# Kernel optimization log

Measured on AMD Instinct MI355X. Metric: run time of the kernel, lower is better.

## Reference

```python
import jax, jax.numpy as jnp
import numpy as np

B, T, F, H = 64, 1024, 512, 512


def setup_inputs() -> dict:
    key = jax.random.key(0)
    k1, k2, k3 = jax.random.split(key, 3)
    scale_x = 1.0 / np.sqrt(F)
    scale_h = 1.0 / np.sqrt(H)
    inputs = jax.random.normal(k1, (B, T, F), dtype=jnp.float32)
    Wx = jax.random.normal(k2, (F, 4 * H), dtype=jnp.float32) * scale_x
    Wh = jax.random.normal(k3, (H, 4 * H), dtype=jnp.float32) * scale_h
    # flax LSTMCell inits forget-gate bias to ones, others zero (gate order i,f,g,o)
    b = jnp.concatenate([jnp.zeros((H,)), jnp.ones((H,)), jnp.zeros((2 * H,))]).astype(jnp.float32)
    return {"inputs": inputs, "Wx": Wx, "Wh": Wh, "b": b}


def reference(inputs, Wx, Wh, b):
    """LSTM encoder: scan LSTMCell over time, return final carry (c, h).

    inputs: [B, T, F]; Wx: [F, 4H]; Wh: [H, 4H]; b: [4H].
    Gate order i, f, g, o (matches flax.nn.LSTMCell).
    """
    Bx = inputs.shape[0]
    Hh = Wh.shape[0]
    # Precompute input projections for all timesteps in one big GEMM: [T, B, 4H]
    x_proj = jnp.einsum('btf,fg->tbg', inputs, Wx) + b

    def step(carry, xp_t):
        c, h = carry
        gates = xp_t + h @ Wh  # [B, 4H]
        i, f, g, o = jnp.split(gates, 4, axis=-1)
        i = jax.nn.sigmoid(i)
        f = jax.nn.sigmoid(f)
        g = jnp.tanh(g)
        o = jax.nn.sigmoid(o)
        c_new = f * c + i * g
        h_new = o * jnp.tanh(c_new)
        return (c_new, h_new), None

    c0 = jnp.zeros((Bx, Hh), dtype=inputs.dtype)
    h0 = jnp.zeros((Bx, Hh), dtype=inputs.dtype)
    (c_fin, h_fin), _ = jax.lax.scan(step, (c0, h0), x_proj)
    return c_fin, h_fin
```

## Files before the change

kernel.cpp:

```cpp
#include <hip/hip_runtime.h>
#include <hip/hip_fp16.h>

#define T_DIM 1024
#define B_DIM 64
#define F_DIM 512
#define H_DIM 512
#define G4    2048
#define HSZ   (B_DIM*H_DIM)

typedef _Float16 h16;
typedef unsigned long long u64;
typedef _Float16 v8h __attribute__((ext_vector_type(8)));
typedef _Float16 v4h __attribute__((ext_vector_type(4)));
typedef _Float16 v2h __attribute__((ext_vector_type(2)));
typedef float    v4f __attribute__((ext_vector_type(4)));
typedef unsigned v4u __attribute__((ext_vector_type(4)));
typedef unsigned v2u __attribute__((ext_vector_type(2)));

#define NGRP   8
#define GROWS  8
#define GWORDS 2048
#define NWG    128
#define DESC_OFF  ((size_t)2*NGRP*GWORDS)
#define TRIAL_OFF (DESC_OFF + NWG)
#define VOTE_OFF  (TRIAL_OFF + NWG)
#define ABORT_OFF (VOTE_OFF + NWG)

#define XP_HALVES ((size_t)T_DIM * 256 * 2 * 64 * 4)
#define XP_BYTES  (XP_HALVES * 2)
#define HB_WORDS  (ABORT_OFF + NGRP)
#define HB_BYTES  (HB_WORDS * 8)
#define X16_BYTES ((size_t)B_DIM * T_DIM * F_DIM * 2)
#define WXP_BYTES ((size_t)G4 * F_DIM * 2)

__global__ __launch_bounds__(256) void conv_x_kernel(
    const float* __restrict__ X, h16* __restrict__ X16)
{
  const size_t total4 = (size_t)B_DIM * T_DIM * F_DIM / 4;
  for (size_t i = blockIdx.x * 256 + threadIdx.x; i < total4;
       i += (size_t)gridDim.x * 256) {
    float4 v = ((const float4*)X)[i];
    v4h w = { (h16)v.x, (h16)v.y, (h16)v.z, (h16)v.w };
    ((v4h*)X16)[i] = w;
  }
}

__global__ __launch_bounds__(256) void conv_w_kernel(
    const float* __restrict__ Wx, h16* __restrict__ Wxp)
{
  const int gid = blockIdx.x * 256 + threadIdx.x;
  const int pcg = gid >> 6;
  const int k8  = gid & 63;
  const int ub  = pcg >> 5, Tt = (pcg >> 4) & 1, nn = pcg & 15;
  const int gcol = (Tt*2 + (nn >> 3))*512 + ub*8 + (nn & 7);
  v8h w;
  #pragma unroll
  for (int j = 0; j < 8; ++j)
    w[j] = (h16)Wx[(size_t)(k8*8 + j)*G4 + gcol];
  *(v8h*)(Wxp + (size_t)pcg*512 + k8*8) = w;
}

__global__ __launch_bounds__(256) void xproj_kernel(
    const h16* __restrict__ X16, const h16* __restrict__ Wxp,
    const float* __restrict__ bias, h16* __restrict__ xp)
{
  __shared__ __align__(16) h16 As[128*72];
  __shared__ __align__(16) h16 Bs[128*72];
  const int wgid = blockIdx.x;
  const int wgn  = wgid & 15;
  const int bg   = (wgid >> 4) & 3;
  const int t0   = (wgid >> 6) * 8;
  const int tid  = threadIdx.x;
  const int lane = tid & 63;
  const int wv   = tid >> 6;
  const int mh   = wv & 1, nh = wv >> 1;
  const int n    = lane & 15, quad = lane >> 4;

  v4f acc[4][4];
  #pragma unroll
  for (int mi = 0; mi < 4; ++mi)
    #pragma unroll
    for (int ni = 0; ni < 4; ++ni) acc[mi][ni] = {0.f, 0.f, 0.f, 0.f};

  const int m  = tid >> 1;
  const int kh = tid & 1;
  const int abl = m & 15, atl = m >> 4;
  const h16* asrc0 = X16 + ((size_t)(bg*16 + abl)*T_DIM + (t0 + atl))*F_DIM
                         + kh*32;
  const h16* bsrc0 = Wxp + (size_t)(wgn*128 + m)*512 + kh*32;
  h16* adst = As + m*72 + kh*32;
  h16* bdst = Bs + m*72 + kh*32;

  for (int kc = 0; kc < 8; ++kc) {
    __syncthreads();
    {
      const h16* asrc = asrc0 + kc*64;
      const h16* bsrc = bsrc0 + kc*64;
      #pragma unroll
      for (int j = 0; j < 32; j += 8) {
        *(v8h*)(adst + j) = *(const v8h*)(asrc + j);
        *(v8h*)(bdst + j) = *(const v8h*)(bsrc + j);
      }
    }
    __syncthreads();
    #pragma unroll
    for (int kk = 0; kk < 2; ++kk) {
      v8h aF[4], bF[4];
      #pragma unroll
      for (int mi = 0; mi < 4; ++mi)
        aF[mi] = *(const v8h*)(As + ((mh*4 + mi)*16 + n)*72 + kk*32 + quad*8);
      #pragma unroll
      for (int ni = 0; ni < 4; ++ni)
        bF[ni] = *(const v8h*)(Bs + ((nh*4 + ni)*16 + n)*72 + kk*32 + quad*8);
      #pragma unroll
      for (int mi = 0; mi < 4; ++mi)
        #pragma unroll
        for (int ni = 0; ni < 4; ++ni)
          acc[mi][ni] = __builtin_amdgcn_mfma_f32_16x16x32_f16(
              aF[mi], bF[ni], acc[mi][ni], 0, 0, 0);
    }
  }
  #pragma unroll
  for (int ni = 0; ni < 4; ++ni) {
    int pc0  = wgn*128 + (nh*4 + ni)*16;
    int ub   = pc0 >> 5, Tt = (pc0 >> 4) & 1;
    int gcol = (Tt*2 + (n >> 3))*512 + ub*8 + (n & 7);
    float bv = bias[gcol];
    int wg2  = bg*64 + ub;
    #pragma unroll
    for (int mi = 0; mi < 4; ++mi) {
      int t = t0 + mh*4 + mi;
      size_t off = ((((size_t)t*256 + wg2)*2 + Tt)*256) + lane*4;
      v4h o = { (h16)(acc[mi][ni][0] + bv), (h16)(acc[mi][ni][1] + bv),
                (h16)(acc[mi][ni][2] + bv), (h16)(acc[mi][ni][3] + bv) };
      *(v4h*)(xp + off) = o;
    }
  }
}

__device__ __forceinline__ float fsig(float x) {
  return __builtin_amdgcn_rcpf(1.f + __expf(-x));
}
__device__ __forceinline__ float ftanh(float x) {
  return 1.f - 2.f * __builtin_amdgcn_rcpf(__expf(2.f*x) + 1.f);
}

__device__ __forceinline__ u64 load_nt_u64(const u64* p) {
  v2u r;
  asm volatile("global_load_dwordx2 %0, %1, off nt\n\ts_waitcnt vmcnt(0)"
               : "=v"(r) : "v"(p) : "memory");
  return ((u64)r.y << 32) | (u64)r.x;
}

__global__ __launch_bounds__(256, 1) void scan_kernel(
    const float* __restrict__ Wh, const h16* __restrict__ xp,
    u64* __restrict__ hbuf, float* __restrict__ out)
{
  const int bx   = blockIdx.x;
  const int tid  = threadIdx.x;
  const int wv   = tid >> 6;
  const int lane = tid & 63;
  const int n    = lane & 15, quad = lane >> 4;

  __shared__ __align__(16) unsigned hlds[2][2052];
  __shared__ float gbuf[4][16*33];
  __shared__ unsigned char xcds[NWG];
  __shared__ unsigned char pos2bx[NWG];
  __shared__ int sflag[2];

  unsigned xcd;
  asm volatile("s_getreg_b32 %0, hwreg(20, 0, 32)" : "=s"(xcd));
  xcd &= 7u;
  u64* const desc = hbuf + DESC_OFF;
  if (tid == 0)
    __hip_atomic_store(desc + bx, ((u64)0xABu << 56) | (u64)xcd,
                       __ATOMIC_RELAXED, __HIP_MEMORY_SCOPE_AGENT);
  if (tid < NWG) {
    u64 d = __hip_atomic_load(desc + tid, __ATOMIC_RELAXED,
                              __HIP_MEMORY_SCOPE_AGENT);
    while ((unsigned)(d >> 56) != 0xABu) {
      __builtin_amdgcn_s_sleep(1);
      d = __hip_atomic_load(desc + tid, __ATOMIC_RELAXED,
                            __HIP_MEMORY_SCOPE_AGENT);
    }
    xcds[tid] = (unsigned char)(d & 7u);
  }
  if (tid < 4) { hlds[0][2048 + tid] = 0; hlds[1][2048 + tid] = 0; }
  __syncthreads();

  int start = 0, cnt = 0, rank = 0;
  for (int i = 0; i < NWG; ++i) {
    const int x = xcds[i];
    start += (x < (int)xcd) ? 1 : 0;
    cnt   += (x == (int)xcd) ? 1 : 0;
    rank  += (x == (int)xcd && i < bx) ? 1 : 0;
  }
  const int pos = start + rank;
  const int g = pos >> 4, w = pos & 15;
  bool fast = (g*16 >= start) && (g*16 + 16 <= start + cnt);

  if (fast) {
    if (tid < NWG) {
      const int xi = xcds[tid];
      int st = 0, rk = 0;
      for (int i = 0; i < NWG; ++i) {
        const int x = xcds[i];
        st += (x < xi) ? 1 : 0;
        rk += (x == xi && i < tid) ? 1 : 0;
      }
      pos2bx[st + rk] = (unsigned char)tid;
    }
    __syncthreads();
    u64* const trial = hbuf + TRIAL_OFF;
    u64* const vote  = hbuf + VOTE_OFF;
    if (tid == 0)
      __hip_atomic_store(trial + bx, ((u64)0xCDu << 56) | (u64)bx,
                         __ATOMIC_RELAXED, __HIP_MEMORY_SCOPE_WORKGROUP);
    int seen = 1;
    if (tid < 16) {
      const int tb = pos2bx[g*16 + tid];
      const u64 want = ((u64)0xCDu << 56) | (u64)tb;
      seen = 0;
      for (int it = 0; it < 1024; ++it) {
        if (load_nt_u64(trial + tb) == want) { seen = 1; break; }
        __builtin_amdgcn_s_sleep(1);
      }
    }
    if (tid < 64) {
      const int okw = __all(seen);
      if (tid == 0) sflag[0] = okw;
    }
    __syncthreads();
    if (tid == 0)
      __hip_atomic_store(vote + bx, ((u64)0xEFu << 56) | (u64)(sflag[0] & 1),
                         __ATOMIC_RELAXED, __HIP_MEMORY_SCOPE_AGENT);
    int vok = 1;
    if (tid < 16) {
      const int tb = pos2bx[g*16 + tid];
      u64 d = __hip_atomic_load(vote + tb, __ATOMIC_RELAXED,
                                __HIP_MEMORY_SCOPE_AGENT);
      while ((unsigned)(d >> 56) != 0xEFu) {
        __builtin_amdgcn_s_sleep(1);
        d = __hip_atomic_load(vote + tb, __ATOMIC_RELAXED,
                              __HIP_MEMORY_SCOPE_AGENT);
      }
      vok = (int)(d & 1);
    }
    if (tid < 64) {
      const int allv = __all(vok);
      if (tid == 0) sflag[1] = allv;
    }
    __syncthreads();
    fast = (sflag[1] != 0);
  }

  const int ub  = w*4 + wv;
  const int u0  = ub*8;
  const int g01 = n >> 3;
  const int uc  = u0 + (n & 7);

  v8h bF0[16], bF1[16];
  #pragma unroll
  for (int kk = 0; kk < 16; ++kk) {
    const int kb = kk*32 + quad*8;
    v8h f0, f1;
    #pragma unroll
    for (int j = 0; j < 8; ++j) {
      f0[j] = (h16)Wh[(size_t)(kb + j)*G4 + (g01*512 + uc)];
      f1[j] = (h16)Wh[(size_t)(kb + j)*G4 + ((2 + g01)*512 + uc)];
    }
    bF0[kk] = f0; bF1[kk] = f1;
  }

  float c0 = 0.f, c1 = 0.f, hf0 = 0.f, hf1 = 0.f;

  const bool act = (n < GROWS);
  const int  pW  = ub*32 + n*4 + quad;
  u64* const gbase0 = hbuf + (size_t)g * GWORDS;
  u64* const gbase1 = hbuf + (size_t)(NGRP + g) * GWORDS;
  u64* const abw    = hbuf + ABORT_OFF + g;
  u64* const gb0p   = gbase0 + pW;
  u64* const gb1p   = gbase1 + pW;
  u64 lw0 = 0, lw1 = 0;

  const int bgrp  = g >> 1;
  const int qq    = (g & 1)*2 + (quad & 1);
  const int lanep = n + 16*qq;
  size_t xoff = ((size_t)(bgrp*64 + ub)*2)*256 + lanep*4;
  v4h x0 = *(const v4h*)(xp + xoff);
  v4h x1 = *(const v4h*)(xp + xoff + 256);

  const int hbase = act ? (quad*32 + n*4) : 2048;
  const int hoff  = act ? 128 : 0;

  for (int t = 0; t < T_DIM; ++t) {
    const int p = t & 1;
    v4h nx0 = x0, nx1 = x1;
    const bool pre = (t + 1 < T_DIM);
    bool did_pre = false;
    const size_t nxo = (((size_t)(t+1)*256 + bgrp*64 + ub)*2)*256 + lanep*4;
    if (!fast && pre) {
      nx0 = *(const v4h*)(xp + nxo);
      nx1 = *(const v4h*)(xp + nxo + 256);
      did_pre = true;
    }

    u64* const hb = (p ? gbase1 : gbase0) + tid*2;
    const unsigned target = (unsigned)t;
    unsigned pay0, pay1, pay2, pay3, pay4, pay5, pay6, pay7;
    bool got = false;

    if (fast) {
      const u64* a0 = hb;
      const u64* a1 = hb + 512;
      const u64* a2 = hb + 1024;
      const u64* a3 = hb + 1536;
      int rounds = 0;
      for (;;) {
        v4u q0, q1, q2, q3;
        asm volatile("global_load_dwordx4 %0, %1, off nt"
                     : "=v"(q0) : "v"(a0) : "memory");
        asm volatile("global_load_dwordx4 %0, %1, off nt"
                     : "=v"(q1) : "v"(a1) : "memory");
        asm volatile("global_load_dwordx4 %0, %1, off nt"
                     : "=v"(q2) : "v"(a2) : "memory");
        asm volatile("global_load_dwordx4 %0, %1, off nt"
                     : "=v"(q3) : "v"(a3) : "memory");
        asm volatile("s_waitcnt vmcnt(0)"
                     : "+v"(q0), "+v"(q1), "+v"(q2), "+v"(q3) :: "memory");
        __builtin_amdgcn_sched_barrier(0);
        const unsigned bad = (q0.y ^ target) | (q0.w ^ target)
                           | (q1.y ^ target) | (q1.w ^ target)
                           | (q2.y ^ target) | (q2.w ^ target)
                           | (q3.y ^ target) | (q3.w ^ target);
        if (__all((int)(bad == 0))) {
          pay0 = q0.x; pay1 = q0.z; pay2 = q1.x; pay3 = q1.z;
          pay4 = q2.x; pay5 = q2.z; pay6 = q3.x; pay7 = q3.z;
          got = true;
          break;
        }
        ++rounds;
        if ((rounds & 31) == 16) {
          u64 ab = __hip_atomic_load(abw, __ATOMIC_RELAXED,
                                     __HIP_MEMORY_SCOPE_AGENT);
          if (__any((int)(ab != 0)) || rounds > 512) {
            __hip_atomic_store(abw, (u64)1, __ATOMIC_RELAXED,
                               __HIP_MEMORY_SCOPE_AGENT);
            if (lw0) __hip_atomic_store(gb0p, lw0, __ATOMIC_RELAXED,
                                        __HIP_MEMORY_SCOPE_AGENT);
            if (lw1) __hip_atomic_store(gb1p, lw1, __ATOMIC_RELAXED,
                                        __HIP_MEMORY_SCOPE_AGENT);
            fast = false;
            break;
          }
        }
        __builtin_amdgcn_s_sleep(1);
      }
    }
    if (!got) {
      for (;;) {
        u64 wq[8];
        #pragma unroll
        for (int j = 0; j < 4; ++j) {
          wq[j*2]   = __hip_atomic_load(hb + j*512,     __ATOMIC_RELAXED,
                                        __HIP_MEMORY_SCOPE_AGENT);
          wq[j*2+1] = __hip_atomic_load(hb + j*512 + 1, __ATOMIC_RELAXED,
                                        __HIP_MEMORY_SCOPE_AGENT);
        }
        unsigned bad = 0;
        #pragma unroll
        for (int j = 0; j < 8; ++j)
          bad |= ((unsigned)(wq[j] >> 32)) ^ target;
        if (__all((int)(bad == 0))) {
          pay0 = (unsigned)wq[0]; pay1 = (unsigned)wq[1];
          pay2 = (unsigned)wq[2]; pay3 = (unsigned)wq[3];
          pay4 = (unsigned)wq[4]; pay5 = (unsigned)wq[5];
          pay6 = (unsigned)wq[6]; pay7 = (unsigned)wq[7];
          break;
        }
        __builtin_amdgcn_s_sleep(1);
      }
    }

    {
      v2u* hl = (v2u*)hlds[p];
      hl[tid]       = (v2u){pay0, pay1};
      hl[tid + 256] = (v2u){pay2, pay3};
      hl[tid + 512] = (v2u){pay4, pay5};
      hl[tid + 768] = (v2u){pay6, pay7};
    }
    __syncthreads();

    if (pre && !did_pre) {
      nx0 = *(const v4h*)(xp + nxo);
      nx1 = *(const v4h*)(xp + nxo + 256);
    }

    v4f acc0 = { (float)x0[0], (float)x0[1], (float)x0[2], (float)x0[3] };
    v4f acc1 = { (float)x1[0], (float)x1[1], (float)x1[2], (float)x1[3] };
    v4f acc2 = { 0.f, 0.f, 0.f, 0.f };
    v4f acc3 = { 0.f, 0.f, 0.f, 0.f };
    const unsigned* hfr = &hlds[p][hbase];
    #pragma unroll
    for (int kk = 0; kk < 8; ++kk) {
      v8h a0 = *(const v8h*)(hfr + kk*hoff);
      v8h a1 = *(const v8h*)(hfr + (kk+8)*hoff);
      acc0 = __builtin_amdgcn_mfma_f32_16x16x32_f16(a0, bF0[kk],   acc0, 0,0,0);
      acc1 = __builtin_amdgcn_mfma_f32_16x16x32_f16(a0, bF1[kk],   acc1, 0,0,0);
      acc2 = __builtin_amdgcn_mfma_f32_16x16x32_f16(a1, bF0[kk+8], acc2, 0,0,0);
      acc3 = __builtin_amdgcn_mfma_f32_16x16x32_f16(a1, bF1[kk+8], acc3, 0,0,0);
    }
    acc0 += acc2; acc1 += acc3;

    float* gb = gbuf[wv];
    #pragma unroll
    for (int r = 0; r < 4; ++r) {
      const int row = quad*4 + r;
      gb[row*33 + n]      = acc0[r];
      gb[row*33 + 16 + n] = acc1[r];
    }
    __builtin_amdgcn_wave_barrier();
    const float* gr = gb + n*33;
    const int ua2 = quad*2;
    float gi0 = gr[ua2],   gf0 = gr[8+ua2], gg0 = gr[16+ua2], go0 = gr[24+ua2];
    float gi1 = gr[ua2+1], gf1 = gr[9+ua2], gg1 = gr[17+ua2], go1 = gr[25+ua2];
    __builtin_amdgcn_wave_barrier();

    gi0 = fsig(gi0); gf0 = fsig(gf0); gg0 = ftanh(gg0); go0 = fsig(go0);
    gi1 = fsig(gi1); gf1 = fsig(gf1); gg1 = ftanh(gg1); go1 = fsig(go1);
    c0 = gf0*c0 + gi0*gg0;  hf0 = go0*ftanh(c0);
    c1 = gf1*c1 + gi1*gg1;  hf1 = go1*ftanh(c1);

    if (t < T_DIM - 1 && act) {
      union { v2h v; unsigned u; } pw;
      pw.v = (v2h){ (h16)hf0, (h16)hf1 };
      const u64 word = ((u64)(unsigned)(t + 1) << 32) | (u64)pw.u;
      u64* const hwp = (p ? gbase0 : gbase1) + pW;
      if (fast) {
        __hip_atomic_store(hwp, word, __ATOMIC_RELAXED,
                           __HIP_MEMORY_SCOPE_WORKGROUP);
        if (p) lw0 = word; else lw1 = word;
      } else {
        __hip_atomic_store(hwp, word, __ATOMIC_RELAXED,
                           __HIP_MEMORY_SCOPE_AGENT);
      }
    }
    x0 = nx0; x1 = nx1;
  }

  if (act) {
    float* oc = out + (size_t)(g*GROWS + n)*H_DIM + u0 + quad*2;
    oc[0] = c0; oc[1] = c1;
    oc[HSZ + 0] = hf0; oc[HSZ + 1] = hf1;
  }
}

extern "C" void kernel_launch(void* const* d_in, const int* in_sizes, int n_in,
                              void* d_out, int out_size, void* d_ws, size_t ws_size,
                              hipStream_t stream) {
  const float* X    = (const float*)d_in[0];
  const float* Wx   = (const float*)d_in[1];
  const float* Wh   = (const float*)d_in[2];
  const float* bias = (const float*)d_in[3];
  float* out = (float*)d_out;

  char* ws = (char*)d_ws;
  h16* xp   = (h16*)ws;
  u64* hbuf = (u64*)(ws + XP_BYTES);
  h16* X16  = (h16*)(ws + XP_BYTES + HB_BYTES);
  h16* Wxp  = (h16*)(ws + XP_BYTES + HB_BYTES + X16_BYTES);

  hipMemsetAsync(ws + XP_BYTES, 0, HB_BYTES, stream);

  conv_x_kernel<<<4096, 256, 0, stream>>>(X, X16);
  conv_w_kernel<<<512, 256, 0, stream>>>(Wx, Wxp);
  xproj_kernel<<<8192, 256, 0, stream>>>(X16, Wxp, bias, xp);
  scan_kernel<<<NWG, 256, 0, stream>>>(Wh, xp, hbuf, out);
}
```

Before: 1.894 ms.

## Stage x-projection in LDS in 16-step windows via bulk register loads

Replaces the per-timestep global load of the precomputed input projection with a bulk load of 16 timesteps into registers. These are written to per-wave LDS at the start of each window and read from LDS every step. The aim is to take global memory latency off the serial recurrence's critical path. It also makes the spin-wait on h skip the sleep for the first few polling rounds. This adds 32KB of LDS and register pressure, and the bursty loads may still stall at window boundaries.

Result: slower. 1.998 ms (+5.5%).

```diff
diff --git a/kernel.cpp b/kernel.cpp
--- a/kernel.cpp
+++ b/kernel.cpp
@@ -21,6 +21,7 @@
 #define GROWS  8
 #define GWORDS 2048
 #define NWG    128
+#define WSTEPS 16
 #define DESC_OFF  ((size_t)2*NGRP*GWORDS)
 #define TRIAL_OFF (DESC_OFF + NWG)
 #define VOTE_OFF  (TRIAL_OFF + NWG)
@@ -163,6 +164,7 @@
   const int n    = lane & 15, quad = lane >> 4;
 
   __shared__ __align__(16) unsigned hlds[2][2052];
+  __shared__ __align__(16) unsigned char xs[4*8192];
   __shared__ float gbuf[4][16*33];
   __shared__ unsigned char xcds[NWG];
   __shared__ unsigned char pos2bx[NWG];
@@ -283,27 +285,31 @@
   u64* const gb1p   = gbase1 + pW;
   u64 lw0 = 0, lw1 = 0;
 
-  const int bgrp  = g >> 1;
-  const int qq    = (g & 1)*2 + (quad & 1);
-  const int lanep = n + 16*qq;
-  size_t xoff = ((size_t)(bgrp*64 + ub)*2)*256 + lanep*4;
-  v4h x0 = *(const v4h*)(xp + xoff);
-  v4h x1 = *(const v4h*)(xp + xoff + 256);
+  const int bgrp = g >> 1;
+  const int gp   = g & 1;
+  unsigned char* const xsw = xs + wv*8192;
+
+  int pslot[8], pchunk[8], pk[8];
+  #pragma unroll
+  for (int j = 0; j < 8; ++j) {
+    const int p2 = j*64 + lane;
+    pslot[j]  = p2 >> 5;
+    pchunk[j] = (p2 >> 4) & 1;
+    pk[j]     = p2 & 15;
+  }
+  v4u rg[8];
+  #pragma unroll
+  for (int j = 0; j < 8; ++j) {
+    const size_t ubase = ((size_t)pslot[j]*256 + bgrp*64 + ub)*512;
+    rg[j] = *(const v4u*)(xp + ubase + gp*128 + pchunk[j]*256 + pk[j]*8);
+  }
 
   const int hbase = act ? (quad*32 + n*4) : 2048;
   const int hoff  = act ? 128 : 0;
 
   for (int t = 0; t < T_DIM; ++t) {
     const int p = t & 1;
-    v4h nx0 = x0, nx1 = x1;
-    const bool pre = (t + 1 < T_DIM);
-    bool did_pre = false;
-    const size_t nxo = (((size_t)(t+1)*256 + bgrp*64 + ub)*2)*256 + lanep*4;
-    if (!fast && pre) {
-      nx0 = *(const v4h*)(xp + nxo);
-      nx1 = *(const v4h*)(xp + nxo + 256);
-      did_pre = true;
-    }
+    const int s = t & 15;
 
     u64* const hb = (p ? gbase1 : gbase0) + tid*2;
     const unsigned target = (unsigned)t;
@@ -354,7 +360,7 @@
             break;
           }
         }
-        __builtin_amdgcn_s_sleep(1);
+        if (rounds > 4) __builtin_amdgcn_s_sleep(1);
       }
     }
     if (!got) {
@@ -382,6 +388,12 @@
       }
     }
 
+    if (s == 0) {
+      #pragma unroll
+      for (int j = 0; j < 8; ++j)
+        *(v4u*)(xsw + pslot[j]*512 + pchunk[j]*256 + pk[j]*16) = rg[j];
+    }
+
     {
       v2u* hl = (v2u*)hlds[p];
       hl[tid]       = (v2u){pay0, pay1};
@@ -391,10 +403,9 @@
     }
     __syncthreads();
 
-    if (pre && !did_pre) {
-      nx0 = *(const v4h*)(xp + nxo);
-      nx1 = *(const v4h*)(xp + nxo + 256);
-    }
+    const unsigned char* xb = xsw + s*512 + (quad & 1)*128 + n*8;
+    v4h x0 = *(const v4h*)xb;
+    v4h x1 = *(const v4h*)(xb + 256);
 
     v4f acc0 = { (float)x0[0], (float)x0[1], (float)x0[2], (float)x0[3] };
     v4f acc1 = { (float)x1[0], (float)x1[1], (float)x1[2], (float)x1[3] };
@@ -445,7 +456,15 @@
                            __HIP_MEMORY_SCOPE_AGENT);
       }
     }
-    x0 = nx0; x1 = nx1;
+
+    if (s == WSTEPS - 1 && t + 1 < T_DIM) {
+      const int tw = t + 1;
+      #pragma unroll
+      for (int j = 0; j < 8; ++j) {
+        const size_t ubase = ((size_t)(tw + pslot[j])*256 + bgrp*64 + ub)*512;
+        rg[j] = *(const v4u*)(xp + ubase + gp*128 + pchunk[j]*256 + pk[j]*8);
+      }
+    }
   }
 
   if (act) {
```

## Fuse fp32-to-fp16 input conversion into xproj GEMM and retune scan polling

Applied to the files above, without the earlier changes.

Removes the separate conv_x kernel and its fp16 staging buffer; the xproj GEMM now loads fp32 inputs directly and converts them to fp16 while filling shared memory. This saves one full write and re-read of the large input tensor and one launch, at the cost of doubling global read bytes for the A operand inside the GEMM. Separately, the scan kernel now prefetches the next timestep's projection only after the wait completes, on every path, and skips s_sleep for the first few polling rounds to cut wakeup latency on the per-step barrier.

Result: slower. 2.320 ms (+22.5%).

```diff
diff --git a/kernel.cpp b/kernel.cpp
--- a/kernel.cpp
+++ b/kernel.cpp
@@ -30,20 +30,7 @@
 #define XP_BYTES  (XP_HALVES * 2)
 #define HB_WORDS  (ABORT_OFF + NGRP)
 #define HB_BYTES  (HB_WORDS * 8)
-#define X16_BYTES ((size_t)B_DIM * T_DIM * F_DIM * 2)
 #define WXP_BYTES ((size_t)G4 * F_DIM * 2)
-
-__global__ __launch_bounds__(256) void conv_x_kernel(
-    const float* __restrict__ X, h16* __restrict__ X16)
-{
-  const size_t total4 = (size_t)B_DIM * T_DIM * F_DIM / 4;
-  for (size_t i = blockIdx.x * 256 + threadIdx.x; i < total4;
-       i += (size_t)gridDim.x * 256) {
-    float4 v = ((const float4*)X)[i];
-    v4h w = { (h16)v.x, (h16)v.y, (h16)v.z, (h16)v.w };
-    ((v4h*)X16)[i] = w;
-  }
-}
 
 __global__ __launch_bounds__(256) void conv_w_kernel(
     const float* __restrict__ Wx, h16* __restrict__ Wxp)
@@ -61,7 +48,7 @@
 }
 
 __global__ __launch_bounds__(256) void xproj_kernel(
-    const h16* __restrict__ X16, const h16* __restrict__ Wxp,
+    const float* __restrict__ X, const h16* __restrict__ Wxp,
     const float* __restrict__ bias, h16* __restrict__ xp)
 {
   __shared__ __align__(16) h16 As[128*72];
@@ -85,7 +72,7 @@
   const int m  = tid >> 1;
   const int kh = tid & 1;
   const int abl = m & 15, atl = m >> 4;
-  const h16* asrc0 = X16 + ((size_t)(bg*16 + abl)*T_DIM + (t0 + atl))*F_DIM
+  const float* asrc0 = X + ((size_t)(bg*16 + abl)*T_DIM + (t0 + atl))*F_DIM
                          + kh*32;
   const h16* bsrc0 = Wxp + (size_t)(wgn*128 + m)*512 + kh*32;
   h16* adst = As + m*72 + kh*32;
@@ -94,11 +81,15 @@
   for (int kc = 0; kc < 8; ++kc) {
     __syncthreads();
     {
-      const h16* asrc = asrc0 + kc*64;
-      const h16* bsrc = bsrc0 + kc*64;
+      const float* asrc = asrc0 + kc*64;
+      const h16*   bsrc = bsrc0 + kc*64;
       #pragma unroll
       for (int j = 0; j < 32; j += 8) {
-        *(v8h*)(adst + j) = *(const v8h*)(asrc + j);
+        float4 f0 = *(const float4*)(asrc + j);
+        float4 f1 = *(const float4*)(asrc + j + 4);
+        v8h wa = { (h16)f0.x, (h16)f0.y, (h16)f0.z, (h16)f0.w,
+                   (h16)f1.x, (h16)f1.y, (h16)f1.z, (h16)f1.w };
+        *(v8h*)(adst + j) = wa;
         *(v8h*)(bdst + j) = *(const v8h*)(bsrc + j);
       }
     }
@@ -295,15 +286,6 @@
 
   for (int t = 0; t < T_DIM; ++t) {
     const int p = t & 1;
-    v4h nx0 = x0, nx1 = x1;
-    const bool pre = (t + 1 < T_DIM);
-    bool did_pre = false;
-    const size_t nxo = (((size_t)(t+1)*256 + bgrp*64 + ub)*2)*256 + lanep*4;
-    if (!fast && pre) {
-      nx0 = *(const v4h*)(xp + nxo);
-      nx1 = *(const v4h*)(xp + nxo + 256);
-      did_pre = true;
-    }
 
     u64* const hb = (p ? gbase1 : gbase0) + tid*2;
     const unsigned target = (unsigned)t;
@@ -354,7 +336,7 @@
             break;
           }
         }
-        __builtin_amdgcn_s_sleep(1);
+        if (rounds > 6) __builtin_amdgcn_s_sleep(1);
       }
     }
     if (!got) {
@@ -382,6 +364,13 @@
       }
     }
 
+    v4h nx0 = x0, nx1 = x1;
+    if (t + 1 < T_DIM) {
+      const size_t nxo = (((size_t)(t+1)*256 + bgrp*64 + ub)*2)*256 + lanep*4;
+      nx0 = *(const v4h*)(xp + nxo);
+      nx1 = *(const v4h*)(xp + nxo + 256);
+    }
+
     {
       v2u* hl = (v2u*)hlds[p];
       hl[tid]       = (v2u){pay0, pay1};
@@ -390,11 +379,6 @@
       hl[tid + 768] = (v2u){pay6, pay7};
     }
     __syncthreads();
-
-    if (pre && !did_pre) {
-      nx0 = *(const v4h*)(xp + nxo);
-      nx1 = *(const v4h*)(xp + nxo + 256);
-    }
 
     v4f acc0 = { (float)x0[0], (float)x0[1], (float)x0[2], (float)x0[3] };
     v4f acc1 = { (float)x1[0], (float)x1[1], (float)x1[2], (float)x1[3] };
@@ -467,13 +451,11 @@
   char* ws = (char*)d_ws;
   h16* xp   = (h16*)ws;
   u64* hbuf = (u64*)(ws + XP_BYTES);
-  h16* X16  = (h16*)(ws + XP_BYTES + HB_BYTES);
-  h16* Wxp  = (h16*)(ws + XP_BYTES + HB_BYTES + X16_BYTES);
+  h16* Wxp  = (h16*)(ws + XP_BYTES + HB_BYTES);
 
   hipMemsetAsync(ws + XP_BYTES, 0, HB_BYTES, stream);
 
-  conv_x_kernel<<<4096, 256, 0, stream>>>(X, X16);
   conv_w_kernel<<<512, 256, 0, stream>>>(Wx, Wxp);
-  xproj_kernel<<<8192, 256, 0, stream>>>(X16, Wxp, bias, xp);
+  xproj_kernel<<<8192, 256, 0, stream>>>(X, Wxp, bias, xp);
   scan_kernel<<<NWG, 256, 0, stream>>>(Wh, xp, hbuf, out);
 }
```

## Transpose recurrent MFMA so gates land in registers, dropping LDS gate shuffle

Applied to the files above, without the earlier changes.

Swaps the MFMA operand roles so Wh columns (permuted so each lane's 4 accumulator rows are i,f,g,o of one unit) form the A operand and h forms B. This removes the per-step LDS round trip through gbuf and the two wave barriers. The x-projection kernel, weight packing and xp layout are rearranged to match. The next-step xp prefetch is moved after the barrier, and the sleep in the fast spin loop is skipped for the first rounds, trading more polling traffic for lower wakeup latency.

After: 1.794 ms. 5.3% less time.

```diff
diff --git a/kernel.cpp b/kernel.cpp
--- a/kernel.cpp
+++ b/kernel.cpp
@@ -26,7 +26,7 @@
 #define VOTE_OFF  (TRIAL_OFF + NWG)
 #define ABORT_OFF (VOTE_OFF + NWG)
 
-#define XP_HALVES ((size_t)T_DIM * 256 * 2 * 64 * 4)
+#define XP_HALVES ((size_t)T_DIM * 512 * 64 * 4)
 #define XP_BYTES  (XP_HALVES * 2)
 #define HB_WORDS  (ABORT_OFF + NGRP)
 #define HB_BYTES  (HB_WORDS * 8)
@@ -51,8 +51,10 @@
   const int gid = blockIdx.x * 256 + threadIdx.x;
   const int pcg = gid >> 6;
   const int k8  = gid & 63;
-  const int ub  = pcg >> 5, Tt = (pcg >> 4) & 1, nn = pcg & 15;
-  const int gcol = (Tt*2 + (nn >> 3))*512 + ub*8 + (nn & 7);
+  const int Mt  = pcg >> 4, mrow = pcg & 15;
+  const int ub  = Mt >> 1, par = Mt & 1;
+  const int ul  = mrow >> 2, gate = mrow & 3;
+  const int gcol = gate*512 + ub*8 + 2*ul + par;
   v8h w;
   #pragma unroll
   for (int j = 0; j < 8; ++j)
@@ -84,10 +86,10 @@
 
   const int m  = tid >> 1;
   const int kh = tid & 1;
-  const int abl = m & 15, atl = m >> 4;
-  const h16* asrc0 = X16 + ((size_t)(bg*16 + abl)*T_DIM + (t0 + atl))*F_DIM
+  const int bbl = m & 15, btl = m >> 4;
+  const h16* asrc0 = Wxp + (size_t)(wgn*128 + m)*512 + kh*32;
+  const h16* bsrc0 = X16 + ((size_t)(bg*16 + bbl)*T_DIM + (t0 + btl))*F_DIM
                          + kh*32;
-  const h16* bsrc0 = Wxp + (size_t)(wgn*128 + m)*512 + kh*32;
   h16* adst = As + m*72 + kh*32;
   h16* bdst = Bs + m*72 + kh*32;
 
@@ -121,18 +123,18 @@
     }
   }
   #pragma unroll
-  for (int ni = 0; ni < 4; ++ni) {
-    int pc0  = wgn*128 + (nh*4 + ni)*16;
-    int ub   = pc0 >> 5, Tt = (pc0 >> 4) & 1;
-    int gcol = (Tt*2 + (n >> 3))*512 + ub*8 + (n & 7);
-    float bv = bias[gcol];
-    int wg2  = bg*64 + ub;
+  for (int mi = 0; mi < 4; ++mi) {
+    const int Mg  = wgn*8 + mh*4 + mi;
+    const int ub  = Mg >> 1, par = Mg & 1;
+    const int unit = ub*8 + 2*quad + par;
+    v4f bv = { bias[unit], bias[512 + unit],
+               bias[1024 + unit], bias[1536 + unit] };
     #pragma unroll
-    for (int mi = 0; mi < 4; ++mi) {
-      int t = t0 + mh*4 + mi;
-      size_t off = ((((size_t)t*256 + wg2)*2 + Tt)*256) + lane*4;
-      v4h o = { (h16)(acc[mi][ni][0] + bv), (h16)(acc[mi][ni][1] + bv),
-                (h16)(acc[mi][ni][2] + bv), (h16)(acc[mi][ni][3] + bv) };
+    for (int ni = 0; ni < 4; ++ni) {
+      const int t = t0 + nh*4 + ni;
+      size_t off = (((size_t)t*512 + bg*128 + Mg)*64 + quad*16 + n)*4;
+      v4h o = { (h16)(acc[mi][ni][0] + bv[0]), (h16)(acc[mi][ni][1] + bv[1]),
+                (h16)(acc[mi][ni][2] + bv[2]), (h16)(acc[mi][ni][3] + bv[3]) };
       *(v4h*)(xp + off) = o;
     }
   }
@@ -163,7 +165,6 @@
   const int n    = lane & 15, quad = lane >> 4;
 
   __shared__ __align__(16) unsigned hlds[2][2052];
-  __shared__ float gbuf[4][16*33];
   __shared__ unsigned char xcds[NWG];
   __shared__ unsigned char pos2bx[NWG];
   __shared__ int sflag[2];
@@ -254,28 +255,30 @@
     fast = (sflag[1] != 0);
   }
 
-  const int ub  = w*4 + wv;
-  const int u0  = ub*8;
-  const int g01 = n >> 3;
-  const int uc  = u0 + (n & 7);
-
-  v8h bF0[16], bF1[16];
-  #pragma unroll
-  for (int kk = 0; kk < 16; ++kk) {
-    const int kb = kk*32 + quad*8;
-    v8h f0, f1;
+  const int ub = w*4 + wv;
+  const int u0 = ub*8;
+
+  v8h whF0[16], whF1[16];
+  {
+    const int gate = n & 3, ul = n >> 2;
+    const int ce = gate*512 + u0 + 2*ul;
     #pragma unroll
-    for (int j = 0; j < 8; ++j) {
-      f0[j] = (h16)Wh[(size_t)(kb + j)*G4 + (g01*512 + uc)];
-      f1[j] = (h16)Wh[(size_t)(kb + j)*G4 + ((2 + g01)*512 + uc)];
-    }
-    bF0[kk] = f0; bF1[kk] = f1;
+    for (int kk = 0; kk < 16; ++kk) {
+      const int kb = kk*32 + quad*8;
+      v8h f0, f1;
+      #pragma unroll
+      for (int j = 0; j < 8; ++j) {
+        f0[j] = (h16)Wh[(size_t)(kb + j)*G4 + ce];
+        f1[j] = (h16)Wh[(size_t)(kb + j)*G4 + ce + 1];
+      }
+      whF0[kk] = f0; whF1[kk] = f1;
+    }
   }
 
   float c0 = 0.f, c1 = 0.f, hf0 = 0.f, hf1 = 0.f;
 
   const bool act = (n < GROWS);
-  const int  pW  = ub*32 + n*4 + quad;
+  const int  pW  = w*128 + wv*32 + n*4 + quad;
   u64* const gbase0 = hbuf + (size_t)g * GWORDS;
   u64* const gbase1 = hbuf + (size_t)(NGRP + g) * GWORDS;
   u64* const abw    = hbuf + ABORT_OFF + g;
@@ -284,9 +287,9 @@
   u64 lw0 = 0, lw1 = 0;
 
   const int bgrp  = g >> 1;
-  const int qq    = (g & 1)*2 + (quad & 1);
-  const int lanep = n + 16*qq;
-  size_t xoff = ((size_t)(bgrp*64 + ub)*2)*256 + lanep*4;
+  const int ghalf = (g & 1)*8;
+  const int lpos  = quad*16 + ghalf + n;
+  size_t xoff = (((size_t)bgrp*128 + ub*2)*64 + lpos)*4;
   v4h x0 = *(const v4h*)(xp + xoff);
   v4h x1 = *(const v4h*)(xp + xoff + 256);
 
@@ -295,15 +298,6 @@
 
   for (int t = 0; t < T_DIM; ++t) {
     const int p = t & 1;
-    v4h nx0 = x0, nx1 = x1;
-    const bool pre = (t + 1 < T_DIM);
-    bool did_pre = false;
-    const size_t nxo = (((size_t)(t+1)*256 + bgrp*64 + ub)*2)*256 + lanep*4;
-    if (!fast && pre) {
-      nx0 = *(const v4h*)(xp + nxo);
-      nx1 = *(const v4h*)(xp + nxo + 256);
-      did_pre = true;
-    }
 
     u64* const hb = (p ? gbase1 : gbase0) + tid*2;
     const unsigned target = (unsigned)t;
@@ -354,7 +348,7 @@
             break;
           }
         }
-        __builtin_amdgcn_s_sleep(1);
+        if (rounds > 6) __builtin_amdgcn_s_sleep(1);
       }
     }
     if (!got) {
@@ -391,7 +385,9 @@
     }
     __syncthreads();
 
-    if (pre && !did_pre) {
+    v4h nx0 = x0, nx1 = x1;
+    if (t + 1 < T_DIM) {
+      const size_t nxo = (((size_t)(t+1)*512 + bgrp*128 + ub*2)*64 + lpos)*4;
       nx0 = *(const v4h*)(xp + nxo);
       nx1 = *(const v4h*)(xp + nxo + 256);
     }
@@ -403,31 +399,19 @@
     const unsigned* hfr = &hlds[p][hbase];
     #pragma unroll
     for (int kk = 0; kk < 8; ++kk) {
-      v8h a0 = *(const v8h*)(hfr + kk*hoff);
-      v8h a1 = *(const v8h*)(hfr + (kk+8)*hoff);
-      acc0 = __builtin_amdgcn_mfma_f32_16x16x32_f16(a0, bF0[kk],   acc0, 0,0,0);
-      acc1 = __builtin_amdgcn_mfma_f32_16x16x32_f16(a0, bF1[kk],   acc1, 0,0,0);
-      acc2 = __builtin_amdgcn_mfma_f32_16x16x32_f16(a1, bF0[kk+8], acc2, 0,0,0);
-      acc3 = __builtin_amdgcn_mfma_f32_16x16x32_f16(a1, bF1[kk+8], acc3, 0,0,0);
+      v8h b0 = *(const v8h*)(hfr + kk*hoff);
+      v8h b1 = *(const v8h*)(hfr + (kk+8)*hoff);
+      acc0 = __builtin_amdgcn_mfma_f32_16x16x32_f16(whF0[kk],   b0, acc0, 0,0,0);
+      acc1 = __builtin_amdgcn_mfma_f32_16x16x32_f16(whF1[kk],   b0, acc1, 0,0,0);
+      acc2 = __builtin_amdgcn_mfma_f32_16x16x32_f16(whF0[kk+8], b1, acc2, 0,0,0);
+      acc3 = __builtin_amdgcn_mfma_f32_16x16x32_f16(whF1[kk+8], b1, acc3, 0,0,0);
     }
     acc0 += acc2; acc1 += acc3;
 
-    float* gb = gbuf[wv];
-    #pragma unroll
-    for (int r = 0; r < 4; ++r) {
-      const int row = quad*4 + r;
-      gb[row*33 + n]      = acc0[r];
-      gb[row*33 + 16 + n] = acc1[r];
-    }
-    __builtin_amdgcn_wave_barrier();
-    const float* gr = gb + n*33;
-    const int ua2 = quad*2;
-    float gi0 = gr[ua2],   gf0 = gr[8+ua2], gg0 = gr[16+ua2], go0 = gr[24+ua2];
-    float gi1 = gr[ua2+1], gf1 = gr[9+ua2], gg1 = gr[17+ua2], go1 = gr[25+ua2];
-    __builtin_amdgcn_wave_barrier();
-
-    gi0 = fsig(gi0); gf0 = fsig(gf0); gg0 = ftanh(gg0); go0 = fsig(go0);
-    gi1 = fsig(gi1); gf1 = fsig(gf1); gg1 = ftanh(gg1); go1 = fsig(go1);
+    float gi0 = fsig(acc0[0]),  gf0 = fsig(acc0[1]);
+    float gg0 = ftanh(acc0[2]), go0 = fsig(acc0[3]);
+    float gi1 = fsig(acc1[0]),  gf1 = fsig(acc1[1]);
+    float gg1 = ftanh(acc1[2]), go1 = fsig(acc1[3]);
     c0 = gf0*c0 + gi0*gg0;  hf0 = go0*ftanh(c0);
     c1 = gf1*c1 + gi1*gg1;  hf1 = go1*ftanh(c1);
 
```
